# Performance work log

Hardware: AMD Instinct MI355X
Metric: run time of the kernel (lower is better)

Reference implementation:

```python
import jax, jax.numpy as jnp
import numpy as np
import math

D_MODEL = 2048
N_HEADS = 16
HEAD_DIM = 128
ROPE_THETA = 10000.0


def apply_rope(x, pos, theta=ROPE_THETA):
    # x: [b, h, s, d], pos: [b, s] int
    d = x.shape[-1]
    inv_freq = 1.0 / (theta ** (jnp.arange(0, d, 2, dtype=jnp.float32) / d))  # [d/2]
    ang = pos.astype(jnp.float32)[:, None, :, None] * inv_freq  # [b,1,s,d/2]
    cos, sin = jnp.cos(ang), jnp.sin(ang)
    x1, x2 = x[..., 0::2], x[..., 1::2]
    out_even = x1 * cos - x2 * sin
    out_odd = x1 * sin + x2 * cos
    return jnp.stack([out_even, out_odd], axis=-1).reshape(x.shape)


def setup_inputs() -> dict:
    key = jax.random.key(0)
    ks = jax.random.split(key, 5)
    b, s = 2, 2048
    scale = 1.0 / math.sqrt(D_MODEL)
    x = jax.random.normal(ks[0], (b, s, D_MODEL), dtype=jnp.float32)
    Wq = jax.random.normal(ks[1], (D_MODEL, D_MODEL), dtype=jnp.float32) * scale
    Wk = jax.random.normal(ks[2], (D_MODEL, D_MODEL), dtype=jnp.float32) * scale
    Wv = jax.random.normal(ks[3], (D_MODEL, D_MODEL), dtype=jnp.float32) * scale
    Wo = jax.random.normal(ks[4], (D_MODEL, D_MODEL), dtype=jnp.float32) * scale
    token_positions = jnp.broadcast_to(jnp.arange(s, dtype=jnp.int32), (b, s))
    return {"x": x, "token_positions": token_positions, "Wq": Wq, "Wk": Wk, "Wv": Wv, "Wo": Wo}


def reference(x, token_positions, Wq, Wk, Wv, Wo):
    b, s, _ = x.shape
    h, d = N_HEADS, HEAD_DIM
    # QKV projections (Linear: x @ W.T), split heads: b s (h d) -> b h s d
    def proj(W):
        y = jnp.einsum('bse,fe->bsf', x, W)
        return y.reshape(b, s, h, d).transpose(0, 2, 1, 3)
    Q, K, V = proj(Wq), proj(Wk), proj(Wv)
    Q = apply_rope(Q, token_positions)
    K = apply_rope(K, token_positions)
    logits = jnp.einsum('bhqd,bhkd->bhqk', Q, K) / math.sqrt(d)
    causal = jnp.triu(jnp.ones((s, s), dtype=bool), 1)
    logits = jnp.where(causal, -jnp.inf, logits)
    attn = jax.nn.softmax(logits, axis=-1)
    ctx = jnp.einsum('bhqk,bhkd->bhqd', attn, V)
    ctx = ctx.transpose(0, 2, 1, 3).reshape(b, s, h * d)
    return jnp.einsum('bsf,ef->bse', ctx, Wo)
```

## Files before the change

kernel.cpp:

```cpp
#include <hip/hip_runtime.h>
#include <cstdint>
#include <cstddef>

typedef __bf16 bf16_t;
typedef __bf16 bf16x8 __attribute__((ext_vector_type(8)));
typedef float  f32x4  __attribute__((ext_vector_type(4)));

#define SEQ 2048
#define NH  16
#define HD  128
#define MM  4096
#define KK  2048

#define ASYNC16(g, l) __builtin_amdgcn_global_load_lds( \
    (const __attribute__((address_space(1))) void*)(g), \
    (__attribute__((address_space(3))) void*)(l), 16, 0, 0)

__global__ __launch_bounds__(256) void cast_all(const float* __restrict__ x,
                                                const float* __restrict__ Wq,
                                                const float* __restrict__ Wk,
                                                const float* __restrict__ Wv,
                                                const float* __restrict__ Wo,
                                                bf16_t* __restrict__ xb,
                                                bf16_t* __restrict__ wqkv,
                                                bf16_t* __restrict__ wob) {
    int i = blockIdx.x * 256 + threadIdx.x;
    const float* src;
    bf16_t* dst;
    int off;
    if (i < 2097152) { src = x; dst = xb; off = i; }
    else {
        int j = i - 2097152;
        int sel = j >> 20; off = j & 0xFFFFF;
        if (sel < 3) { src = (sel == 0) ? Wq : (sel == 1) ? Wk : Wv; dst = wqkv + (size_t)sel * 4194304; }
        else         { src = Wo; dst = wob; }
    }
    float4 v = ((const float4*)src)[off];
    union { bf16_t h[4]; uint2 u; } t;
    t.h[0] = (bf16_t)v.x; t.h[1] = (bf16_t)v.y;
    t.h[2] = (bf16_t)v.z; t.h[3] = (bf16_t)v.w;
    ((uint2*)dst)[off] = t.u;
}

union SMemU {
    struct { bf16_t A[2][4096]; bf16_t B[2][4096]; } st;
    bf16_t epi[64 * 136];
};

template<int MODE>
__device__ __forceinline__ void gemm_body(SMemU& sm,
                                          const bf16_t* __restrict__ A,
                                          const bf16_t* __restrict__ B,
                                          void* __restrict__ Cout,
                                          bf16_t* __restrict__ Kout,
                                          bf16_t* __restrict__ Vout,
                                          const int* __restrict__ pos) {
    const int tid = threadIdx.x;
    const int w = tid >> 6, l = tid & 63;
    const int lane16 = l & 15, quad = l >> 4;
    const int tm = blockIdx.y, tn = blockIdx.x;
    const int wm = w >> 1, wn = w & 1;

    const bf16_t* pA0 = A + (size_t)(tm * 128 + (2 * w + 0) * 16 + lane16) * KK + quad * 8;
    const bf16_t* pA1 = A + (size_t)(tm * 128 + (2 * w + 1) * 16 + lane16) * KK + quad * 8;
    const bf16_t* pB0 = B + (size_t)(tn * 128 + (2 * w + 0) * 16 + lane16) * KK + quad * 8;
    const bf16_t* pB1 = B + (size_t)(tn * 128 + (2 * w + 1) * 16 + lane16) * KK + quad * 8;

    f32x4 acc[4][4];
    for (int i = 0; i < 4; i++)
        for (int j = 0; j < 4; j++) acc[i][j] = (f32x4){0.f, 0.f, 0.f, 0.f};

    ASYNC16(pA0, &sm.st.A[0][(2 * w + 0) * 512]);
    ASYNC16(pA1, &sm.st.A[0][(2 * w + 1) * 512]);
    ASYNC16(pB0, &sm.st.B[0][(2 * w + 0) * 512]);
    ASYNC16(pB1, &sm.st.B[0][(2 * w + 1) * 512]);

    int cur = 0;
    for (int k0 = 0; k0 < KK; k0 += 32) {
        __syncthreads();
        if (k0 + 32 < KK) {
            const int nbuf = 1 - cur;
            ASYNC16(pA0 + 32, &sm.st.A[nbuf][(2 * w + 0) * 512]);
            ASYNC16(pA1 + 32, &sm.st.A[nbuf][(2 * w + 1) * 512]);
            ASYNC16(pB0 + 32, &sm.st.B[nbuf][(2 * w + 0) * 512]);
            ASYNC16(pB1 + 32, &sm.st.B[nbuf][(2 * w + 1) * 512]);
            pA0 += 32; pA1 += 32; pB0 += 32; pB1 += 32;
        }
        const bf16_t* rA = &sm.st.A[cur][wm * 2048 + l * 8];
        const bf16_t* rB = &sm.st.B[cur][wn * 2048 + l * 8];
        bf16x8 af[4], bfr[4];
        for (int i = 0; i < 4; i++) af[i]  = *(const bf16x8*)(rA + i * 512);
        for (int j = 0; j < 4; j++) bfr[j] = *(const bf16x8*)(rB + j * 512);
        for (int i = 0; i < 4; i++)
            for (int j = 0; j < 4; j++)
                acc[i][j] = __builtin_amdgcn_mfma_f32_16x16x32_bf16(af[i], bfr[j], acc[i][j], 0, 0, 0);
        cur ^= 1;
    }

    if (MODE == 1) {
        const int mbase = tm * 128 + wm * 64;
        const int nbase = tn * 128 + wn * 64;
        for (int i = 0; i < 4; i++)
            for (int j = 0; j < 4; j++) {
                const int n  = nbase + j * 16 + lane16;
                const int m0 = mbase + i * 16 + quad * 4;
                for (int r = 0; r < 4; r++)
                    ((float*)Cout)[(size_t)(m0 + r) * 2048 + n] = acc[i][j][r];
            }
        return;
    }

    const int mbase = tm * 128;
    const int nb    = tn * 128;
    const int sel   = nb >> 11;
    const int hh    = (nb & 2047) >> 7;
    const int bidx  = mbase >> 11;
    const int g  = tid >> 4;
    const int c8 = (tid & 15) * 8;

    if (sel < 2) {
        bf16_t* dstbase = ((sel == 0) ? (bf16_t*)Cout : Kout) +
                          (size_t)(bidx * NH + hh) * SEQ * HD;
        const float qs = (sel == 0) ? 0.08838834764831845f : 1.0f;
        for (int half = 0; half < 2; half++) {
            __syncthreads();
            if (wm == half) {
                for (int i = 0; i < 4; i++)
                    for (int j = 0; j < 4; j++)
                        for (int r = 0; r < 4; r++)
                            sm.epi[(i * 16 + quad * 4 + r) * 136 + wn * 64 + j * 16 + lane16] =
                                (bf16_t)acc[i][j][r];
            }
            __syncthreads();
            for (int p = 0; p < 4; p++) {
                const int rid = p * 16 + g;
                const int s = (mbase & 2047) + half * 64 + rid;
                bf16x8 v = *(const bf16x8*)&sm.epi[rid * 136 + c8];
                const float pp = (float)pos[bidx * SEQ + s];
                union { bf16_t h8[8]; uint4 u; } o;
                for (int t = 0; t < 4; t++) {
                    const int fi = (c8 >> 1) + t;
                    const float freq = exp2f(-(float)fi * 0.20762050593045857f);
                    const float ang = pp * freq;
                    const float sn = __sinf(ang), cs = __cosf(ang);
                    const float x1 = (float)v[2 * t], x2 = (float)v[2 * t + 1];
                    o.h8[2 * t]     = (bf16_t)((x1 * cs - x2 * sn) * qs);
                    o.h8[2 * t + 1] = (bf16_t)((x1 * sn + x2 * cs) * qs);
                }
                *(uint4*)(dstbase + (size_t)s * HD + c8) = o.u;
            }
        }
    } else {
        bf16_t* dstb = Vout + (size_t)(bidx * NH + hh) * HD * SEQ;
        const int s0 = mbase & 2047;
        for (int half = 0; half < 2; half++) {
            __syncthreads();
            if (wn == half) {
                for (int i = 0; i < 4; i++)
                    for (int j = 0; j < 4; j++) {
                        union { bf16_t h4[4]; uint2 u; } pk;
                        for (int r = 0; r < 4; r++) pk.h4[r] = (bf16_t)acc[i][j][r];
                        *(uint2*)&sm.epi[(j * 16 + lane16) * 136 + wm * 64 + i * 16 + quad * 4] = pk.u;
                    }
            }
            __syncthreads();
            for (int p = 0; p < 4; p++) {
                const int rid = p * 16 + g;
                const int d = half * 64 + rid;
                bf16x8 v = *(const bf16x8*)&sm.epi[rid * 136 + c8];
                *(uint4*)(dstb + (size_t)d * SEQ + s0 + c8) = *(const uint4*)&v;
            }
        }
    }
}

__global__ __launch_bounds__(256) void gemm_qkv(const bf16_t* __restrict__ A,
                                                const bf16_t* __restrict__ B,
                                                bf16_t* __restrict__ Qout,
                                                bf16_t* __restrict__ Kout,
                                                bf16_t* __restrict__ Vout,
                                                const int* __restrict__ pos) {
    __shared__ SMemU sm;
    gemm_body<3>(sm, A, B, (void*)Qout, Kout, Vout, pos);
}

__global__ __launch_bounds__(256) void gemm_out(const bf16_t* __restrict__ A,
                                                const bf16_t* __restrict__ B,
                                                float* __restrict__ Cout) {
    __shared__ SMemU sm;
    gemm_body<1>(sm, A, B, (void*)Cout, nullptr, nullptr, nullptr);
}

__global__ __launch_bounds__(256) void attn_kernel(const bf16_t* __restrict__ Q,
                                                   const bf16_t* __restrict__ K,
                                                   const bf16_t* __restrict__ Vt,
                                                   bf16_t* __restrict__ ctx) {
    const int flat = blockIdx.x;
    const int bh = flat & 31;
    const int bt = flat >> 5;
    const int h = bh & 15, b = bh >> 4;
    const bf16_t* Qh = Q  + (size_t)bh * SEQ * HD;
    const bf16_t* Kh = K  + (size_t)bh * SEQ * HD;
    const bf16_t* Vh = Vt + (size_t)bh * HD * SEQ;

    const int tid = threadIdx.x;
    const int w = tid >> 6, l = tid & 63;
    const int lane16 = l & 15, quad = l >> 4;

    __shared__ bf16_t kt[2][16 * 512];
    __shared__ bf16_t vt[2][16 * 512];
    __shared__ bf16_t pbuf[4][1024];

    for (int half = 0; half < 2; half++) {
        const int qt = half ? (31 - bt) : bt;
        const int q0 = qt * 64 + w * 16;

        bf16x8 qf[4];
        {
            const bf16_t* qrow = Qh + (size_t)(q0 + lane16) * HD + quad * 8;
            for (int kc = 0; kc < 4; kc++) qf[kc] = *(const bf16x8*)(qrow + kc * 32);
        }

        f32x4 o[8];
        for (int dt = 0; dt < 8; dt++) o[dt] = (f32x4){0.f, 0.f, 0.f, 0.f};
        float m_s = -INFINITY, l_s = 0.f;

        __syncthreads();
        for (int ii = 0; ii < 4; ii++) {
            const int f = w * 4 + ii;
            const int nt = f >> 2, kc = f & 3;
            ASYNC16(Kh + (size_t)(nt * 16 + lane16) * HD + kc * 32 + quad * 8, &kt[0][f * 512]);
            const int dt = f >> 1, kk = f & 1;
            ASYNC16(Vh + (size_t)(dt * 16 + lane16) * SEQ + kk * 32 + quad * 8, &vt[0][f * 512]);
        }

        int cur = 0;
        for (int kb = 0; kb <= qt; kb++) {
            const int k0 = kb * 64;
            __syncthreads();
            if (kb < qt) {
                const int kn = k0 + 64;
                for (int ii = 0; ii < 4; ii++) {
                    const int f = w * 4 + ii;
                    const int nt = f >> 2, kc = f & 3;
                    ASYNC16(Kh + (size_t)(kn + nt * 16 + lane16) * HD + kc * 32 + quad * 8,
                            &kt[1 - cur][f * 512]);
                    const int dt = f >> 1, kk = f & 1;
                    ASYNC16(Vh + (size_t)(dt * 16 + lane16) * SEQ + kn + kk * 32 + quad * 8,
                            &vt[1 - cur][f * 512]);
                }
            }
            const bf16_t* ktc = kt[cur];
            const bf16_t* vtc = vt[cur];

            f32x4 sacc[4];
            for (int nt = 0; nt < 4; nt++) sacc[nt] = (f32x4){0.f, 0.f, 0.f, 0.f};
            __builtin_amdgcn_s_setprio(1);
            for (int nt = 0; nt < 4; nt++)
                for (int kc = 0; kc < 4; kc++) {
                    bf16x8 kf = *(const bf16x8*)&ktc[(nt * 4 + kc) * 512 + l * 8];
                    sacc[nt] = __builtin_amdgcn_mfma_f32_16x16x32_bf16(kf, qf[kc], sacc[nt], 0, 0, 0);
                }
            __builtin_amdgcn_s_setprio(0);
            if (kb == qt) {
                const int qg = q0 + lane16;
                for (int nt = 0; nt < 4; nt++)
                    for (int r = 0; r < 4; r++) {
                        const int kg = k0 + nt * 16 + quad * 4 + r;
                        if (kg > qg) sacc[nt][r] = -INFINITY;
                    }
            }
            float rmnt[4];
            for (int nt = 0; nt < 4; nt++)
                rmnt[nt] = fmaxf(fmaxf(sacc[nt][0], sacc[nt][1]),
                                 fmaxf(sacc[nt][2], sacc[nt][3]));
            float rowmax = fmaxf(fmaxf(rmnt[0], rmnt[1]), fmaxf(rmnt[2], rmnt[3]));
            rowmax = fmaxf(rowmax, __shfl_xor(rowmax, 16, 64));
            rowmax = fmaxf(rowmax, __shfl_xor(rowmax, 32, 64));

            float a = 1.f;
            const bool noresc = __all(rowmax <= m_s + 8.f) != 0;
            if (!noresc) {
                const float mnew = fmaxf(m_s, rowmax);
                a = __expf(m_s - mnew);
                m_s = mnew;
            }
            float ssum = 0.f;
            for (int nt = 0; nt < 4; nt++) {
                union { bf16_t h4[4]; uint2 u; } pk;
                for (int r = 0; r < 4; r++) {
                    const float e = __expf(sacc[nt][r] - m_s);
                    ssum += e;
                    pk.h4[r] = (bf16_t)e;
                }
                const int addr = (nt >> 1) * 512 +
                                 (((nt & 1) * 2 + (quad >> 1)) * 16 + lane16) * 8 +
                                 (quad & 1) * 4;
                *(uint2*)&pbuf[w][addr] = pk.u;
            }
            ssum += __shfl_xor(ssum, 16, 64);
            ssum += __shfl_xor(ssum, 32, 64);
            l_s = l_s * a + ssum;

            if (!noresc) {
                float ar[4];
                for (int r = 0; r < 4; r++) ar[r] = __shfl(a, (quad << 2) | r, 16);
                for (int dt = 0; dt < 8; dt++)
                    for (int r = 0; r < 4; r++) o[dt][r] *= ar[r];
            }
            __builtin_amdgcn_s_setprio(1);
            for (int kk = 0; kk < 2; kk++) {
                bf16x8 pf = *(const bf16x8*)&pbuf[w][kk * 512 + l * 8];
                for (int dt = 0; dt < 8; dt++) {
                    bf16x8 vf = *(const bf16x8*)&vtc[(dt * 2 + kk) * 512 + l * 8];
                    o[dt] = __builtin_amdgcn_mfma_f32_16x16x32_bf16(pf, vf, o[dt], 0, 0, 0);
                }
            }
            __builtin_amdgcn_s_setprio(0);
            cur ^= 1;
        }

        float inv[4];
        for (int r = 0; r < 4; r++) inv[r] = 1.0f / __shfl(l_s, (quad << 2) | r, 16);
        for (int r = 0; r < 4; r++) {
            const int qg = q0 + quad * 4 + r;
            bf16_t* dst = ctx + ((size_t)(b * SEQ + qg)) * (NH * HD) + h * HD;
            for (int dt = 0; dt < 8; dt++)
                dst[dt * 16 + lane16] = (bf16_t)(o[dt][r] * inv[r]);
        }
        __syncthreads();
    }
}

extern "C" void kernel_launch(void* const* d_in, const int* in_sizes, int n_in,
                              void* d_out, int out_size, void* d_ws, size_t ws_size,
                              hipStream_t stream) {
    const float* x  = (const float*)d_in[0];
    const int* pos  = (const int*)d_in[1];
    const float* Wq = (const float*)d_in[2];
    const float* Wk = (const float*)d_in[3];
    const float* Wv = (const float*)d_in[4];
    const float* Wo = (const float*)d_in[5];

    char* ws = (char*)d_ws;
    bf16_t* xb   = (bf16_t*)(ws);
    bf16_t* wqkv = (bf16_t*)(ws + (16u << 20));
    bf16_t* wob  = (bf16_t*)(ws + (40u << 20));
    bf16_t* Qb   = (bf16_t*)(ws + (48u << 20));
    bf16_t* Kb   = (bf16_t*)(ws + (64u << 20));
    bf16_t* Vt   = (bf16_t*)(ws + (80u << 20));
    bf16_t* ctx  = (bf16_t*)(ws + (96u << 20));

    cast_all<<<24576, 256, 0, stream>>>(x, Wq, Wk, Wv, Wo, xb, wqkv, wob);

    dim3 gq(6144 / 128, MM / 128);
    gemm_qkv<<<gq, 256, 0, stream>>>(xb, wqkv, Qb, Kb, Vt, pos);

    attn_kernel<<<512, 256, 0, stream>>>(Qb, Kb, Vt, ctx);

    dim3 gg(2048 / 128, MM / 128);
    gemm_out<<<gg, 256, 0, stream>>>(ctx, wob, (float*)d_out);
}
```

Before: 468.2 us.

## Triple-buffer GEMM LDS staging with explicit vmcnt waits for deeper prefetch

Moves the GEMM main loop from double to triple buffering in LDS, keeping two k-tiles in flight. An explicit s_waitcnt vmcnt(4) plus a raw s_barrier replaces __syncthreads, so the wait covers only the oldest outstanding tile. The aim is to hide more global-load latency behind MFMA work. In exchange LDS use rises from 32KB to 48KB per block, which may lower occupancy, and the code now depends on the exact count of outstanding vm loads.

Result: faster. 455.1 us (-2.8%).

```diff
diff --git a/kernel.cpp b/kernel.cpp
--- a/kernel.cpp
+++ b/kernel.cpp
@@ -43,7 +43,7 @@
 }
 
 union SMemU {
-    struct { bf16_t A[2][4096]; bf16_t B[2][4096]; } st;
+    struct { bf16_t A[3][4096]; bf16_t B[3][4096]; } st;
     bf16_t epi[64 * 136];
 };
 
@@ -70,31 +70,44 @@
     for (int i = 0; i < 4; i++)
         for (int j = 0; j < 4; j++) acc[i][j] = (f32x4){0.f, 0.f, 0.f, 0.f};
 
-    ASYNC16(pA0, &sm.st.A[0][(2 * w + 0) * 512]);
-    ASYNC16(pA1, &sm.st.A[0][(2 * w + 1) * 512]);
-    ASYNC16(pB0, &sm.st.B[0][(2 * w + 0) * 512]);
-    ASYNC16(pB1, &sm.st.B[0][(2 * w + 1) * 512]);
-
-    int cur = 0;
-    for (int k0 = 0; k0 < KK; k0 += 32) {
-        __syncthreads();
-        if (k0 + 32 < KK) {
-            const int nbuf = 1 - cur;
-            ASYNC16(pA0 + 32, &sm.st.A[nbuf][(2 * w + 0) * 512]);
-            ASYNC16(pA1 + 32, &sm.st.A[nbuf][(2 * w + 1) * 512]);
-            ASYNC16(pB0 + 32, &sm.st.B[nbuf][(2 * w + 0) * 512]);
-            ASYNC16(pB1 + 32, &sm.st.B[nbuf][(2 * w + 1) * 512]);
-            pA0 += 32; pA1 += 32; pB0 += 32; pB1 += 32;
-        }
-        const bf16_t* rA = &sm.st.A[cur][wm * 2048 + l * 8];
-        const bf16_t* rB = &sm.st.B[cur][wn * 2048 + l * 8];
+    ASYNC16(pA0,      &sm.st.A[0][(2 * w + 0) * 512]);
+    ASYNC16(pA1,      &sm.st.A[0][(2 * w + 1) * 512]);
+    ASYNC16(pB0,      &sm.st.B[0][(2 * w + 0) * 512]);
+    ASYNC16(pB1,      &sm.st.B[0][(2 * w + 1) * 512]);
+    ASYNC16(pA0 + 32, &sm.st.A[1][(2 * w + 0) * 512]);
+    ASYNC16(pA1 + 32, &sm.st.A[1][(2 * w + 1) * 512]);
+    ASYNC16(pB0 + 32, &sm.st.B[1][(2 * w + 0) * 512]);
+    ASYNC16(pB1 + 32, &sm.st.B[1][(2 * w + 1) * 512]);
+
+    const bf16_t* qA0 = pA0 + 64;
+    const bf16_t* qA1 = pA1 + 64;
+    const bf16_t* qB0 = pB0 + 64;
+    const bf16_t* qB1 = pB1 + 64;
+
+    const int NT = KK / 32;
+    int rdbuf = 0, stbuf = 2;
+    for (int t = 0; t < NT; ++t) {
+        if (t == NT - 1) { asm volatile("s_waitcnt vmcnt(0) lgkmcnt(0)" ::: "memory"); }
+        else             { asm volatile("s_waitcnt vmcnt(4) lgkmcnt(0)" ::: "memory"); }
+        __builtin_amdgcn_s_barrier();
+        asm volatile("" ::: "memory");
+        if (t + 2 < NT) {
+            ASYNC16(qA0, &sm.st.A[stbuf][(2 * w + 0) * 512]);
+            ASYNC16(qA1, &sm.st.A[stbuf][(2 * w + 1) * 512]);
+            ASYNC16(qB0, &sm.st.B[stbuf][(2 * w + 0) * 512]);
+            ASYNC16(qB1, &sm.st.B[stbuf][(2 * w + 1) * 512]);
+            qA0 += 32; qA1 += 32; qB0 += 32; qB1 += 32;
+            stbuf = (stbuf == 2) ? 0 : stbuf + 1;
+        }
+        const bf16_t* rA = &sm.st.A[rdbuf][wm * 2048 + l * 8];
+        const bf16_t* rB = &sm.st.B[rdbuf][wn * 2048 + l * 8];
         bf16x8 af[4], bfr[4];
         for (int i = 0; i < 4; i++) af[i]  = *(const bf16x8*)(rA + i * 512);
         for (int j = 0; j < 4; j++) bfr[j] = *(const bf16x8*)(rB + j * 512);
         for (int i = 0; i < 4; i++)
             for (int j = 0; j < 4; j++)
                 acc[i][j] = __builtin_amdgcn_mfma_f32_16x16x32_bf16(af[i], bfr[j], acc[i][j], 0, 0, 0);
-        cur ^= 1;
+        rdbuf = (rdbuf == 2) ? 0 : rdbuf + 1;
     }
 
     if (MODE == 1) {
```
